# Performance work log

Hardware: AMD Instinct MI355X
Metric: run time of the kernel (lower is better)

The kernel has to match this reference:

```python
import jax, jax.numpy as jnp
import numpy as np

B, S, E, H, NQ = 8, 2048, 8, 2, 8
D = E // H  # head_dim = 4
DIM = 2 ** NQ  # 256-amplitude state vector

# CNOT chain pattern from the module: (0,1),(1,2),...,(NQ-2,NQ-1),(NQ-1,0)
CNOTS = [(i, i + 1) for i in range(NQ - 1)] + [(NQ - 1, 0)]

# Pauli-Z sign table: wire 0 is the most-significant qubit axis (torchquantum convention)
_k = np.arange(DIM)
_SIGNS = (1.0 - 2.0 * ((_k[None, :] >> (NQ - 1 - np.arange(NQ))[:, None]) & 1)).astype(np.float32)  # (NQ, DIM)


def _quantum_measure(tok):
    """Batched simulation of the per-token circuit. tok: (N, E) real -> (N, NQ) <Z> values."""
    n = tok.shape[0]
    idx = jnp.arange(NQ) % D
    # encoder RX(tok[w]) then explicit RX(tok[w % head_dim]) on each wire: angles add.
    half = 0.5 * (tok[:, :NQ] + tok[:, idx])  # (N, NQ)
    a0 = jnp.cos(half).astype(jnp.complex64)
    a1 = (-1j) * jnp.sin(half).astype(jnp.complex64)
    qub = jnp.stack([a0, a1], axis=-1)  # (N, NQ, 2) per-qubit states (product state before CNOTs)
    # Kronecker product across the fixed NQ wires
    state = qub[:, 0, :]
    for w in range(1, NQ):
        state = (state[:, :, None] * qub[:, w, None, :]).reshape(n, -1)
    state = state.reshape((n,) + (2,) * NQ)
    # CNOT chain: flip target axis within control=1 block
    for c, t in CNOTS:
        c0 = jax.lax.index_in_dim(state, 0, c + 1, keepdims=True)
        c1 = jnp.flip(jax.lax.index_in_dim(state, 1, c + 1, keepdims=True), axis=t + 1)
        state = jnp.concatenate([c0, c1], axis=c + 1)
    p = (state.real ** 2 + state.imag ** 2).reshape(n, DIM)  # probabilities
    return p @ jnp.asarray(_SIGNS.T)  # (N, NQ) Pauli-Z expectations


def setup_inputs() -> dict:
    key = jax.random.key(0)
    ks = jax.random.split(key, 5)
    sc = 1.0 / np.sqrt(E)
    return {
        "x": jax.random.normal(ks[0], (B, S, E), jnp.float32),
        "Wq": jax.random.normal(ks[1], (E, E), jnp.float32) * sc,
        "Wk": jax.random.normal(ks[2], (E, E), jnp.float32) * sc,
        "Wv": jax.random.normal(ks[3], (E, E), jnp.float32) * sc,
        "Wo": jax.random.normal(ks[4], (E, E), jnp.float32) * sc,
    }


def reference(x, Wq, Wk, Wv, Wo):
    b, s, _ = x.shape
    # nn.Linear(bias=False): y = x @ W^T
    q = jnp.einsum('bse,fe->bsf', x, Wq).reshape(b, s, H, D)
    k = jnp.einsum('bse,fe->bsf', x, Wk).reshape(b, s, H, D)
    v = jnp.einsum('bse,fe->bsf', x, Wv).reshape(b, s, H, D)
    scores = jnp.einsum('bihd,bjhd->bhij', q, k) / jnp.sqrt(jnp.float32(D))
    attn = jax.nn.softmax(scores, axis=-1)  # dropout is identity at inference
    out = jnp.einsum('bhij,bjhd->bihd', attn, v).reshape(b, s, E)
    z = _quantum_measure(out.reshape(-1, E)).reshape(b, s, NQ)  # NQ == E
    return jnp.einsum('bsq,fq->bsf', z, Wo)
```

## Files before the change

### kernel.cpp

```cpp
#include <hip/hip_runtime.h>


#define SS 2048
#define EE 8

extern "C" __global__ __launch_bounds__(512)
void qa_attn(const float* __restrict__ x, const float* __restrict__ Wq,
             const float* __restrict__ Wk, const float* __restrict__ Wv,
             float* __restrict__ AO) {
    __shared__ __align__(16) char smem[65536];
    float4* kv4  = (float4*)smem;
    float*  pden = (float*)smem;
    float4* pacc = (float4*)(smem + 2048 * 4);

    const int bid = blockIdx.x;
    const int rb  = bid & 31;
    const int h   = (bid >> 5) & 1;
    const int b   = bid >> 6;
    const int tid = threadIdx.x;
    const int hoff = h * 4;

    #pragma unroll
    for (int u = 0; u < 4; ++u) {
        const int j = tid + u * 512;
        const float* xp = x + ((size_t)(b * SS + j)) * EE;
        float4 x0 = *(const float4*)xp;
        float4 x1 = *(const float4*)(xp + 4);
        float xv[8] = {x0.x, x0.y, x0.z, x0.w, x1.x, x1.y, x1.z, x1.w};
        float kk[4], vv[4];
        #pragma unroll
        for (int d = 0; d < 4; ++d) {
            const float* wkr = Wk + (hoff + d) * EE;
            const float* wvr = Wv + (hoff + d) * EE;
            float sk = 0.f, sv = 0.f;
            #pragma unroll
            for (int e = 0; e < 8; ++e) { sk += xv[e] * wkr[e]; sv += xv[e] * wvr[e]; }
            kk[d] = sk; vv[d] = sv;
        }
        kv4[j * 2]     = make_float4(kk[0], kk[1], kk[2], kk[3]);
        kv4[j * 2 + 1] = make_float4(vv[0], vv[1], vv[2], vv[3]);
    }

    const int r  = tid & 63;
    const int sl = tid >> 6;
    const int i  = rb * 64 + r;
    float q[4];
    {
        const float* xp = x + ((size_t)(b * SS + i)) * EE;
        float4 x0 = *(const float4*)xp;
        float4 x1 = *(const float4*)(xp + 4);
        float xv[8] = {x0.x, x0.y, x0.z, x0.w, x1.x, x1.y, x1.z, x1.w};
        #pragma unroll
        for (int d = 0; d < 4; ++d) {
            const float* wqr = Wq + (hoff + d) * EE;
            float s = 0.f;
            #pragma unroll
            for (int e = 0; e < 8; ++e) s += xv[e] * wqr[e];
            q[d] = s;
        }
    }
    __syncthreads();

    float den = 0.f, a0 = 0.f, a1 = 0.f, a2 = 0.f, a3 = 0.f;
    const int j0 = sl * 256;
    #pragma unroll 4
    for (int j = j0; j < j0 + 256; ++j) {
        float4 kk = kv4[j * 2];
        float4 vv = kv4[j * 2 + 1];
        float s = 0.5f * (q[0] * kk.x + q[1] * kk.y + q[2] * kk.z + q[3] * kk.w);
        float e = __expf(s);
        den += e;
        a0 += e * vv.x; a1 += e * vv.y; a2 += e * vv.z; a3 += e * vv.w;
    }

    __syncthreads();
    pden[sl * 64 + r] = den;
    pacc[sl * 64 + r] = make_float4(a0, a1, a2, a3);
    __syncthreads();
    if (sl == 0) {
        #pragma unroll
        for (int u = 1; u < 8; ++u) {
            den += pden[u * 64 + r];
            float4 p = pacc[u * 64 + r];
            a0 += p.x; a1 += p.y; a2 += p.z; a3 += p.w;
        }
        const float inv = 1.f / den;
        *(float4*)(AO + (((size_t)(b * SS + i)) * 2 + h) * 4) =
            make_float4(a0 * inv, a1 * inv, a2 * inv, a3 * inv);
    }
}

extern "C" __global__ __launch_bounds__(256)
void qa_quantum(const float* __restrict__ AO, const float* __restrict__ Wo,
                float* __restrict__ out) {
    __shared__ float wo[64];
    const int tid = threadIdx.x;
    if (tid < 64) wo[tid] = Wo[tid];
    __syncthreads();

    const int g = blockIdx.x * 256 + tid;
    const float* tp = AO + (size_t)g * 8;
    float4 t0 = *(const float4*)tp;
    float4 t1 = *(const float4*)(tp + 4);
    float tok[8] = {t0.x, t0.y, t0.z, t0.w, t1.x, t1.y, t1.z, t1.w};

    float c[8];
    #pragma unroll
    for (int w = 0; w < 8; ++w) c[w] = __cosf(tok[w] + tok[w & 3]);

    float z[8];
    float p = 1.f;
    #pragma unroll
    for (int qq = 1; qq < 8; ++qq) { p *= c[qq]; z[qq] = p; }
    z[0] = p;
    #pragma unroll
    for (int qq = 1; qq < 8; ++qq) z[qq] *= c[0];

    float y[8];
    #pragma unroll
    for (int f = 0; f < 8; ++f) {
        float s = 0.f;
        #pragma unroll
        for (int qq = 0; qq < 8; ++qq) s += z[qq] * wo[f * 8 + qq];
        y[f] = s;
    }
    float* op = out + (size_t)g * 8;
    *(float4*)op       = make_float4(y[0], y[1], y[2], y[3]);
    *(float4*)(op + 4) = make_float4(y[4], y[5], y[6], y[7]);
}

extern "C" void kernel_launch(void* const* d_in, const int* in_sizes, int n_in,
                              void* d_out, int out_size, void* d_ws, size_t ws_size,
                              hipStream_t stream) {
    const float* x  = (const float*)d_in[0];
    const float* Wq = (const float*)d_in[1];
    const float* Wk = (const float*)d_in[2];
    const float* Wv = (const float*)d_in[3];
    const float* Wo = (const float*)d_in[4];
    float* out = (float*)d_out;
    float* AO  = (float*)d_ws;

    qa_attn<<<dim3(512), dim3(512), 0, stream>>>(x, Wq, Wk, Wv, AO);
    qa_quantum<<<dim3(64), dim3(256), 0, stream>>>(AO, Wo, out);
}
```

Before: 91.12 us.

## Register-tile attention with readlane K/V broadcast and split-KV partials

Rewrites the attention kernel so each thread holds four query rows in registers. Each lane computes its own key and value rows, which are broadcast across the wavefront with readlane, so the shared-memory K/V staging goes away. The key axis is split across blocks and waves, and partial denominators and accumulators go to a workspace. The quantum kernel reduces those partials. The softmax scale is folded into Wq with log2(e) so that exp2 can be used directly. This removes LDS bandwidth and the per-block recomputation of all 2048 K/V rows, at the cost of more global partial traffic, a larger workspace and heavy register use.

After: 96.04 us. 5.4% more time.

```diff
diff --git a/kernel.cpp b/kernel.cpp
--- a/kernel.cpp
+++ b/kernel.cpp
@@ -4,109 +4,123 @@
 #define SS 2048
 #define EE 8
 
-extern "C" __global__ __launch_bounds__(512)
-void qa_attn(const float* __restrict__ x, const float* __restrict__ Wq,
-             const float* __restrict__ Wk, const float* __restrict__ Wv,
-             float* __restrict__ AO) {
-    __shared__ __align__(16) char smem[65536];
-    float4* kv4  = (float4*)smem;
-    float*  pden = (float*)smem;
-    float4* pacc = (float4*)(smem + 2048 * 4);
+__device__ __forceinline__ float rl(float v, int t) {
+    return __int_as_float(__builtin_amdgcn_readlane(__float_as_int(v), t));
+}
 
+extern "C" __global__ __launch_bounds__(256)
+void qa_attn2(const float* __restrict__ x, const float* __restrict__ Wq,
+              const float* __restrict__ Wk, const float* __restrict__ Wv,
+              float* __restrict__ wsD, float4* __restrict__ wsA) {
+    __shared__ float wrow[96];
     const int bid = blockIdx.x;
-    const int rb  = bid & 31;
-    const int h   = (bid >> 5) & 1;
-    const int b   = bid >> 6;
-    const int tid = threadIdx.x;
-    const int hoff = h * 4;
+    const int jq = bid & 3, rt = (bid >> 2) & 7, h = (bid >> 5) & 1, b = bid >> 6;
+    const int tid = threadIdx.x, lane = tid & 63, w = tid >> 6;
 
-    #pragma unroll
-    for (int u = 0; u < 4; ++u) {
-        const int j = tid + u * 512;
-        const float* xp = x + ((size_t)(b * SS + j)) * EE;
-        float4 x0 = *(const float4*)xp;
-        float4 x1 = *(const float4*)(xp + 4);
-        float xv[8] = {x0.x, x0.y, x0.z, x0.w, x1.x, x1.y, x1.z, x1.w};
-        float kk[4], vv[4];
-        #pragma unroll
-        for (int d = 0; d < 4; ++d) {
-            const float* wkr = Wk + (hoff + d) * EE;
-            const float* wvr = Wv + (hoff + d) * EE;
-            float sk = 0.f, sv = 0.f;
-            #pragma unroll
-            for (int e = 0; e < 8; ++e) { sk += xv[e] * wkr[e]; sv += xv[e] * wvr[e]; }
-            kk[d] = sk; vv[d] = sv;
-        }
-        kv4[j * 2]     = make_float4(kk[0], kk[1], kk[2], kk[3]);
-        kv4[j * 2 + 1] = make_float4(vv[0], vv[1], vv[2], vv[3]);
-    }
-
-    const int r  = tid & 63;
-    const int sl = tid >> 6;
-    const int i  = rb * 64 + r;
-    float q[4];
-    {
-        const float* xp = x + ((size_t)(b * SS + i)) * EE;
-        float4 x0 = *(const float4*)xp;
-        float4 x1 = *(const float4*)(xp + 4);
-        float xv[8] = {x0.x, x0.y, x0.z, x0.w, x1.x, x1.y, x1.z, x1.w};
-        #pragma unroll
-        for (int d = 0; d < 4; ++d) {
-            const float* wqr = Wq + (hoff + d) * EE;
-            float s = 0.f;
-            #pragma unroll
-            for (int e = 0; e < 8; ++e) s += xv[e] * wqr[e];
-            q[d] = s;
-        }
+    if (tid < 96) {
+        const int grp = tid >> 5, d = (tid >> 3) & 3, e = tid & 7;
+        const float* W = (grp == 0) ? Wq : (grp == 1 ? Wk : Wv);
+        float val = W[(h * 4 + d) * EE + e];
+        if (grp == 0) val *= 0.72134752044f;
+        wrow[tid] = val;
     }
     __syncthreads();
 
-    float den = 0.f, a0 = 0.f, a1 = 0.f, a2 = 0.f, a3 = 0.f;
-    const int j0 = sl * 256;
-    #pragma unroll 4
-    for (int j = j0; j < j0 + 256; ++j) {
-        float4 kk = kv4[j * 2];
-        float4 vv = kv4[j * 2 + 1];
-        float s = 0.5f * (q[0] * kk.x + q[1] * kk.y + q[2] * kk.z + q[3] * kk.w);
-        float e = __expf(s);
-        den += e;
-        a0 += e * vv.x; a1 += e * vv.y; a2 += e * vv.z; a3 += e * vv.w;
+    float q[4][4];
+    const int row0 = rt * 256 + lane;
+    #pragma unroll
+    for (int m = 0; m < 4; ++m) {
+        const float* xp = x + ((size_t)(b * SS + row0 + m * 64)) * EE;
+        float xv[8];
+        *(float4*)&xv[0] = *(const float4*)xp;
+        *(float4*)&xv[4] = *(const float4*)(xp + 4);
+        #pragma unroll
+        for (int d = 0; d < 4; ++d) {
+            float s = 0.f;
+            #pragma unroll
+            for (int e = 0; e < 8; ++e) s += xv[e] * wrow[d * 8 + e];
+            q[m][d] = s;
+        }
     }
 
-    __syncthreads();
-    pden[sl * 64 + r] = den;
-    pacc[sl * 64 + r] = make_float4(a0, a1, a2, a3);
-    __syncthreads();
-    if (sl == 0) {
+    float den[4] = {0.f, 0.f, 0.f, 0.f};
+    float acc[4][4] = {};
+
+    const int jbase = jq * 512 + w * 128;
+    #pragma unroll 1
+    for (int g = 0; g < 2; ++g) {
+        const int myj = jbase + g * 64 + lane;
+        const float* xp = x + ((size_t)(b * SS + myj)) * EE;
+        float xv[8];
+        *(float4*)&xv[0] = *(const float4*)xp;
+        *(float4*)&xv[4] = *(const float4*)(xp + 4);
+        float mk[4], mv[4];
         #pragma unroll
-        for (int u = 1; u < 8; ++u) {
-            den += pden[u * 64 + r];
-            float4 p = pacc[u * 64 + r];
-            a0 += p.x; a1 += p.y; a2 += p.z; a3 += p.w;
+        for (int d = 0; d < 4; ++d) {
+            float sk = 0.f, sv = 0.f;
+            #pragma unroll
+            for (int e = 0; e < 8; ++e) {
+                sk += xv[e] * wrow[32 + d * 8 + e];
+                sv += xv[e] * wrow[64 + d * 8 + e];
+            }
+            mk[d] = sk; mv[d] = sv;
         }
-        const float inv = 1.f / den;
-        *(float4*)(AO + (((size_t)(b * SS + i)) * 2 + h) * 4) =
-            make_float4(a0 * inv, a1 * inv, a2 * inv, a3 * inv);
+        #pragma unroll 16
+        for (int t = 0; t < 64; ++t) {
+            const float k0 = rl(mk[0], t), k1 = rl(mk[1], t),
+                        k2 = rl(mk[2], t), k3 = rl(mk[3], t);
+            const float v0 = rl(mv[0], t), v1 = rl(mv[1], t),
+                        v2 = rl(mv[2], t), v3 = rl(mv[3], t);
+            #pragma unroll
+            for (int m = 0; m < 4; ++m) {
+                const float s = q[m][0] * k0 + q[m][1] * k1 + q[m][2] * k2 + q[m][3] * k3;
+                const float e = __builtin_amdgcn_exp2f(s);
+                den[m] += e;
+                acc[m][0] += e * v0; acc[m][1] += e * v1;
+                acc[m][2] += e * v2; acc[m][3] += e * v3;
+            }
+        }
+    }
+
+    const int slice = jq * 4 + w;
+    #pragma unroll
+    for (int m = 0; m < 4; ++m) {
+        const size_t idx = ((size_t)((b * 2 + h) * 16 + slice)) * SS + row0 + m * 64;
+        wsD[idx] = den[m];
+        wsA[idx] = make_float4(acc[m][0], acc[m][1], acc[m][2], acc[m][3]);
     }
 }
 
 extern "C" __global__ __launch_bounds__(256)
-void qa_quantum(const float* __restrict__ AO, const float* __restrict__ Wo,
-                float* __restrict__ out) {
+void qa_quantum2(const float* __restrict__ wsD, const float4* __restrict__ wsA,
+                 const float* __restrict__ Wo, float* __restrict__ out) {
     __shared__ float wo[64];
     const int tid = threadIdx.x;
     if (tid < 64) wo[tid] = Wo[tid];
     __syncthreads();
 
     const int g = blockIdx.x * 256 + tid;
-    const float* tp = AO + (size_t)g * 8;
-    float4 t0 = *(const float4*)tp;
-    float4 t1 = *(const float4*)(tp + 4);
-    float tok[8] = {t0.x, t0.y, t0.z, t0.w, t1.x, t1.y, t1.z, t1.w};
+    const int b = g >> 11, s = g & 2047;
+
+    float tok[8];
+    #pragma unroll
+    for (int h = 0; h < 2; ++h) {
+        float den = 0.f, a0 = 0.f, a1 = 0.f, a2 = 0.f, a3 = 0.f;
+        #pragma unroll
+        for (int sl = 0; sl < 16; ++sl) {
+            const size_t idx = ((size_t)((b * 2 + h) * 16 + sl)) * SS + s;
+            den += wsD[idx];
+            const float4 p = wsA[idx];
+            a0 += p.x; a1 += p.y; a2 += p.z; a3 += p.w;
+        }
+        const float inv = 1.f / den;
+        tok[h * 4 + 0] = a0 * inv; tok[h * 4 + 1] = a1 * inv;
+        tok[h * 4 + 2] = a2 * inv; tok[h * 4 + 3] = a3 * inv;
+    }
 
     float c[8];
     #pragma unroll
-    for (int w = 0; w < 8; ++w) c[w] = __cosf(tok[w] + tok[w & 3]);
+    for (int ww = 0; ww < 8; ++ww) c[ww] = __cosf(tok[ww] + tok[ww & 3]);
 
     float z[8];
     float p = 1.f;
@@ -119,10 +133,10 @@
     float y[8];
     #pragma unroll
     for (int f = 0; f < 8; ++f) {
-        float s = 0.f;
+        float sum = 0.f;
         #pragma unroll
-        for (int qq = 0; qq < 8; ++qq) s += z[qq] * wo[f * 8 + qq];
-        y[f] = s;
+        for (int qq = 0; qq < 8; ++qq) sum += z[qq] * wo[f * 8 + qq];
+        y[f] = sum;
     }
     float* op = out + (size_t)g * 8;
     *(float4*)op       = make_float4(y[0], y[1], y[2], y[3]);
@@ -138,8 +152,10 @@
     const float* Wv = (const float*)d_in[3];
     const float* Wo = (const float*)d_in[4];
     float* out = (float*)d_out;
-    float* AO  = (float*)d_ws;
 
-    qa_attn<<<dim3(512), dim3(512), 0, stream>>>(x, Wq, Wk, Wv, AO);
-    qa_quantum<<<dim3(64), dim3(256), 0, stream>>>(AO, Wo, out);
+    float*  wsD = (float*)d_ws;
+    float4* wsA = (float4*)((char*)d_ws + (8 * 2 * 16 * 2048) * sizeof(float));
+
+    qa_attn2<<<dim3(512), dim3(256), 0, stream>>>(x, Wq, Wk, Wv, wsD, wsA);
+    qa_quantum2<<<dim3(64), dim3(256), 0, stream>>>(wsD, wsA, Wo, out);
 }
```

## Compute attention scores with fp16 MFMA using precomputed K/V buffers

Applied to the files above, without the earlier changes.

Adds a prep kernel that projects K (packed to fp16 in an MFMA operand layout) and V into global workspace once per batch-head. The attention kernel then computes QK^T scores with 16x16x32 fp16 MFMA instructions, folds the softmax scale and log2e into Q so it can use exp2, and reduces across lanes with shuffles instead of shared-memory partials. This removes the per-block redundant K/V projection and the scalar dot products. In exchange it adds a kernel launch, global traffic for K/V, fp16 precision loss in the scores, and a largely zero-padded MFMA operand.

Result: slower. 135.6 us (+48.9%).

```diff
diff --git a/kernel.cpp b/kernel.cpp
--- a/kernel.cpp
+++ b/kernel.cpp
@@ -4,89 +4,119 @@
 #define SS 2048
 #define EE 8
 
-extern "C" __global__ __launch_bounds__(512)
-void qa_attn(const float* __restrict__ x, const float* __restrict__ Wq,
-             const float* __restrict__ Wk, const float* __restrict__ Wv,
-             float* __restrict__ AO) {
-    __shared__ __align__(16) char smem[65536];
-    float4* kv4  = (float4*)smem;
-    float*  pden = (float*)smem;
-    float4* pacc = (float4*)(smem + 2048 * 4);
+typedef __attribute__((ext_vector_type(8))) _Float16 f16x8;
+typedef __attribute__((ext_vector_type(4))) float f32x4;
 
-    const int bid = blockIdx.x;
-    const int rb  = bid & 31;
-    const int h   = (bid >> 5) & 1;
-    const int b   = bid >> 6;
-    const int tid = threadIdx.x;
-    const int hoff = h * 4;
+union FragU { int4 w; f16x8 v; };
 
-    #pragma unroll
-    for (int u = 0; u < 4; ++u) {
-        const int j = tid + u * 512;
+__device__ __forceinline__ int pkh(float a, float b) {
+    __fp16 __attribute__((ext_vector_type(2))) h = __builtin_amdgcn_cvt_pkrtz(a, b);
+    int r; __builtin_memcpy(&r, &h, 4); return r;
+}
+
+extern "C" __global__ __launch_bounds__(256)
+void qa_prep(const float* __restrict__ x, const float* __restrict__ Wk,
+             const float* __restrict__ Wv,
+             int4* __restrict__ Kimg, float4* __restrict__ Vbuf) {
+    const int gid = blockIdx.x * 256 + threadIdx.x;
+    if (gid < 32768) {
+        const int n = gid & 15, tile = (gid >> 4) & 127, bh = gid >> 11;
+        const int h = bh & 1, b = bh >> 1;
+        const int j = tile * 16 + n;
         const float* xp = x + ((size_t)(b * SS + j)) * EE;
-        float4 x0 = *(const float4*)xp;
-        float4 x1 = *(const float4*)(xp + 4);
-        float xv[8] = {x0.x, x0.y, x0.z, x0.w, x1.x, x1.y, x1.z, x1.w};
-        float kk[4], vv[4];
+        float xv[8];
+        *(float4*)&xv[0] = *(const float4*)xp;
+        *(float4*)&xv[4] = *(const float4*)(xp + 4);
+        float kd[4];
         #pragma unroll
         for (int d = 0; d < 4; ++d) {
-            const float* wkr = Wk + (hoff + d) * EE;
-            const float* wvr = Wv + (hoff + d) * EE;
-            float sk = 0.f, sv = 0.f;
+            float s = 0.f;
             #pragma unroll
-            for (int e = 0; e < 8; ++e) { sk += xv[e] * wkr[e]; sv += xv[e] * wvr[e]; }
-            kk[d] = sk; vv[d] = sv;
+            for (int e = 0; e < 8; ++e) s += xv[e] * Wk[(h * 4 + d) * EE + e];
+            kd[d] = s;
         }
-        kv4[j * 2]     = make_float4(kk[0], kk[1], kk[2], kk[3]);
-        kv4[j * 2 + 1] = make_float4(vv[0], vv[1], vv[2], vv[3]);
+        Kimg[gid] = make_int4(pkh(kd[0], kd[1]), pkh(kd[2], kd[3]), 0, 0);
+    } else {
+        const int vg = gid - 32768;
+        const int j = vg & 2047, bh = vg >> 11;
+        const int h = bh & 1, b = bh >> 1;
+        const float* xp = x + ((size_t)(b * SS + j)) * EE;
+        float xv[8];
+        *(float4*)&xv[0] = *(const float4*)xp;
+        *(float4*)&xv[4] = *(const float4*)(xp + 4);
+        float vd[4];
+        #pragma unroll
+        for (int d = 0; d < 4; ++d) {
+            float s = 0.f;
+            #pragma unroll
+            for (int e = 0; e < 8; ++e) s += xv[e] * Wv[(h * 4 + d) * EE + e];
+            vd[d] = s;
+        }
+        Vbuf[vg] = make_float4(vd[0], vd[1], vd[2], vd[3]);
+    }
+}
+
+extern "C" __global__ __launch_bounds__(256)
+void qa_attn_mf(const float* __restrict__ x, const float* __restrict__ Wq,
+                const int4* __restrict__ Kimg, const float4* __restrict__ Vbuf,
+                float* __restrict__ AO) {
+    const int bid = blockIdx.x;
+    const int rt = bid & 31, h = (bid >> 5) & 1, b = bid >> 6, bh = b * 2 + h;
+    const int tid = threadIdx.x, lane = tid & 63, w = tid >> 6;
+    const int q4 = lane >> 4, n = lane & 15;
+    const int i0 = rt * 64 + w * 16;
+
+    FragU qf; qf.w = make_int4(0, 0, 0, 0);
+    {
+        const float* xp = x + ((size_t)(b * SS + i0 + n)) * EE;
+        float xv[8];
+        *(float4*)&xv[0] = *(const float4*)xp;
+        *(float4*)&xv[4] = *(const float4*)(xp + 4);
+        float qd[4];
+        #pragma unroll
+        for (int d = 0; d < 4; ++d) {
+            float s = 0.f;
+            #pragma unroll
+            for (int e = 0; e < 8; ++e) s += xv[e] * Wq[(h * 4 + d) * EE + e];
+            qd[d] = s * 0.72134752044f;
+        }
+        if (q4 == 0) qf.w = make_int4(pkh(qd[0], qd[1]), pkh(qd[2], qd[3]), 0, 0);
     }
 
-    const int r  = tid & 63;
-    const int sl = tid >> 6;
-    const int i  = rb * 64 + r;
-    float q[4];
-    {
-        const float* xp = x + ((size_t)(b * SS + i)) * EE;
-        float4 x0 = *(const float4*)xp;
-        float4 x1 = *(const float4*)(xp + 4);
-        float xv[8] = {x0.x, x0.y, x0.z, x0.w, x1.x, x1.y, x1.z, x1.w};
-        #pragma unroll
-        for (int d = 0; d < 4; ++d) {
-            const float* wqr = Wq + (hoff + d) * EE;
-            float s = 0.f;
-            #pragma unroll
-            for (int e = 0; e < 8; ++e) s += xv[e] * wqr[e];
-            q[d] = s;
-        }
-    }
-    __syncthreads();
+    const int4*   Kp = Kimg + bh * 2048 + n;
+    const float4* Vp = Vbuf + bh * 2048 + q4 * 4;
 
-    float den = 0.f, a0 = 0.f, a1 = 0.f, a2 = 0.f, a3 = 0.f;
-    const int j0 = sl * 256;
+    float den = 0.f, ac0 = 0.f, ac1 = 0.f, ac2 = 0.f, ac3 = 0.f;
     #pragma unroll 4
-    for (int j = j0; j < j0 + 256; ++j) {
-        float4 kk = kv4[j * 2];
-        float4 vv = kv4[j * 2 + 1];
-        float s = 0.5f * (q[0] * kk.x + q[1] * kk.y + q[2] * kk.z + q[3] * kk.w);
-        float e = __expf(s);
-        den += e;
-        a0 += e * vv.x; a1 += e * vv.y; a2 += e * vv.z; a3 += e * vv.w;
+    for (int t = 0; t < 128; ++t) {
+        FragU kf; kf.w = Kp[t * 16];
+        f32x4 S = __builtin_amdgcn_mfma_f32_16x16x32_f16(
+            kf.v, qf.v, (f32x4){0.f, 0.f, 0.f, 0.f}, 0, 0, 0);
+        const float4 v0 = Vp[t * 16 + 0];
+        const float4 v1 = Vp[t * 16 + 1];
+        const float4 v2 = Vp[t * 16 + 2];
+        const float4 v3 = Vp[t * 16 + 3];
+        const float e0 = __builtin_amdgcn_exp2f(S[0]);
+        const float e1 = __builtin_amdgcn_exp2f(S[1]);
+        const float e2 = __builtin_amdgcn_exp2f(S[2]);
+        const float e3 = __builtin_amdgcn_exp2f(S[3]);
+        den += (e0 + e1) + (e2 + e3);
+        ac0 += fmaf(e0, v0.x, fmaf(e1, v1.x, fmaf(e2, v2.x, e3 * v3.x)));
+        ac1 += fmaf(e0, v0.y, fmaf(e1, v1.y, fmaf(e2, v2.y, e3 * v3.y)));
+        ac2 += fmaf(e0, v0.z, fmaf(e1, v1.z, fmaf(e2, v2.z, e3 * v3.z)));
+        ac3 += fmaf(e0, v0.w, fmaf(e1, v1.w, fmaf(e2, v2.w, e3 * v3.w)));
     }
 
-    __syncthreads();
-    pden[sl * 64 + r] = den;
-    pacc[sl * 64 + r] = make_float4(a0, a1, a2, a3);
-    __syncthreads();
-    if (sl == 0) {
-        #pragma unroll
-        for (int u = 1; u < 8; ++u) {
-            den += pden[u * 64 + r];
-            float4 p = pacc[u * 64 + r];
-            a0 += p.x; a1 += p.y; a2 += p.z; a3 += p.w;
-        }
+    den += __shfl_xor(den, 16); den += __shfl_xor(den, 32);
+    ac0 += __shfl_xor(ac0, 16); ac0 += __shfl_xor(ac0, 32);
+    ac1 += __shfl_xor(ac1, 16); ac1 += __shfl_xor(ac1, 32);
+    ac2 += __shfl_xor(ac2, 16); ac2 += __shfl_xor(ac2, 32);
+    ac3 += __shfl_xor(ac3, 16); ac3 += __shfl_xor(ac3, 32);
+
+    if (lane < 16) {
         const float inv = 1.f / den;
-        *(float4*)(AO + (((size_t)(b * SS + i)) * 2 + h) * 4) =
-            make_float4(a0 * inv, a1 * inv, a2 * inv, a3 * inv);
+        *(float4*)(AO + ((size_t)((b * SS + i0 + n) * 2 + h)) * 4) =
+            make_float4(ac0 * inv, ac1 * inv, ac2 * inv, ac3 * inv);
     }
 }
 
@@ -106,7 +136,7 @@
 
     float c[8];
     #pragma unroll
-    for (int w = 0; w < 8; ++w) c[w] = __cosf(tok[w] + tok[w & 3]);
+    for (int ww = 0; ww < 8; ++ww) c[ww] = __cosf(tok[ww] + tok[ww & 3]);
 
     float z[8];
     float p = 1.f;
@@ -138,8 +168,12 @@
     const float* Wv = (const float*)d_in[3];
     const float* Wo = (const float*)d_in[4];
     float* out = (float*)d_out;
-    float* AO  = (float*)d_ws;
 
-    qa_attn<<<dim3(512), dim3(512), 0, stream>>>(x, Wq, Wk, Wv, AO);
+    int4*   Kimg = (int4*)d_ws;
+    float4* Vbuf = (float4*)((char*)d_ws + (512 << 10));
+    float*  AO   = (float*)((char*)d_ws + (1 << 20));
+
+    qa_prep<<<dim3(256), dim3(256), 0, stream>>>(x, Wk, Wv, Kimg, Vbuf);
+    qa_attn_mf<<<dim3(512), dim3(256), 0, stream>>>(x, Wq, Kimg, Vbuf, AO);
     qa_quantum<<<dim3(64), dim3(256), 0, stream>>>(AO, Wo, out);
 }
```
